# Optimization experiments

Measured on AMD Instinct MI355X. Metric: run time of the kernel, lower is better.

The kernel has to match this reference:

```python
import jax, jax.numpy as jnp
import numpy as np

DIM = 128
BASE = 10000.0
DIM_X = DIM // 2          # 64
DIM_Y = DIM - DIM_X       # 64
H = 512
W = 512


def setup_inputs() -> dict:
    key = jax.random.key(0)
    x = jax.random.normal(key, (1, H * W, DIM), dtype=jnp.float32)
    inv_freq_x = 1.0 / BASE ** (jnp.arange(0, DIM_X, 2, dtype=jnp.float32) / DIM_X)  # [DIM_X//2]
    inv_freq_y = 1.0 / BASE ** (jnp.arange(0, DIM_Y, 2, dtype=jnp.float32) / DIM_Y)  # [DIM_Y//2]
    return {"x": x, "inv_freq_x": inv_freq_x, "inv_freq_y": inv_freq_y,
            "height": H, "width": W}


def reference(x, inv_freq_x, inv_freq_y, height, width):
    dtype = x.dtype
    dim_x = 2 * inv_freq_x.shape[0]
    dim_y = 2 * inv_freq_y.shape[0]
    pos_x = jnp.arange(width, dtype=jnp.float32)   # [W]
    pos_y = jnp.arange(height, dtype=jnp.float32)  # [H]
    freqs_x = pos_x[:, None] * inv_freq_x[None, :]           # [W, dim_x//2]
    freqs_y = pos_y[:, None] * inv_freq_y[None, :]           # [H, dim_y//2]
    freqs_x = jnp.concatenate([freqs_x, freqs_x], axis=-1)   # [W, dim_x]
    freqs_y = jnp.concatenate([freqs_y, freqs_y], axis=-1)   # [H, dim_y]
    # first dim_x channels vary with w (broadcast over y); last dim_y vary with y
    cos_x = jnp.broadcast_to(jnp.cos(freqs_x).astype(dtype)[None, :, :], (height, width, dim_x))
    sin_x = jnp.broadcast_to(jnp.sin(freqs_x).astype(dtype)[None, :, :], (height, width, dim_x))
    cos_y = jnp.broadcast_to(jnp.cos(freqs_y).astype(dtype)[:, None, :], (height, width, dim_y))
    sin_y = jnp.broadcast_to(jnp.sin(freqs_y).astype(dtype)[:, None, :], (height, width, dim_y))
    cos_2d = jnp.concatenate([cos_x, cos_y], axis=-1).reshape(height * width, dim_x + dim_y)
    sin_2d = jnp.concatenate([sin_x, sin_y], axis=-1).reshape(height * width, dim_x + dim_y)
    return cos_2d, sin_2d
```

## Files before the change

kernel.cpp:

```cpp
#include <hip/hip_runtime.h>


typedef __attribute__((ext_vector_type(4))) float float4v;

__global__ __launch_bounds__(256) void rope2d_fast(
    const float* __restrict__ ifx,
    const float* __restrict__ ify,
    const int* __restrict__ wptr,
    float* __restrict__ out,
    int rows)
{
    const int idx = blockIdx.x * blockDim.x + threadIdx.x;
    const int total4 = rows << 6;
    if (idx >= total4) return;

    const int e = idx << 2;
    const int half = rows << 7;
    const bool is_sin = e >= half;
    const int e2 = is_sin ? e - half : e;

    const int p  = e2 >> 7;
    const int ch = e2 & 127;

    const int W = *wptr;
    int xw, yh;
    if ((W & (W - 1)) == 0) {
        const int s = __ffs(W) - 1;
        xw = p & (W - 1);
        yh = p >> s;
    } else {
        xw = p % W;
        yh = p / W;
    }

    const bool use_x = ch < 64;
    const float pos = use_x ? (float)xw : (float)yh;
    const float* tab = use_x ? ifx : ify;
    const float4v fr = *reinterpret_cast<const float4v*>(tab + (ch & 31));

    float4v v;
#pragma unroll
    for (int i = 0; i < 4; ++i) {
        const float f = pos * fr[i];
        v[i] = is_sin ? __sinf(f) : __cosf(f);
    }

    *reinterpret_cast<float4v*>(out + e) = v;
}

__global__ __launch_bounds__(256) void rope2d_generic(
    const float* __restrict__ ifx,
    const float* __restrict__ ify,
    const int* __restrict__ wptr,
    float* __restrict__ out,
    int rows, int dimx, int dimy)
{
    const int dim = dimx + dimy;
    const long long total = 2LL * rows * dim;
    const long long e = (long long)(blockIdx.x * blockDim.x + threadIdx.x);
    if (e >= total) return;

    const long long halfo = (long long)rows * dim;
    const bool is_sin = e >= halfo;
    const long long e2 = is_sin ? e - halfo : e;
    const int p  = (int)(e2 / dim);
    const int ch = (int)(e2 % dim);

    const int W = *wptr;
    const int xw = p % W, yh = p / W;

    float pos, f;
    if (ch < dimx) { pos = (float)xw; f = ifx[ch % (dimx >> 1)]; }
    else           { pos = (float)yh; f = ify[(ch - dimx) % (dimy >> 1)]; }
    const float ang = pos * f;
    out[e] = is_sin ? __sinf(ang) : __cosf(ang);
}

extern "C" void kernel_launch(void* const* d_in, const int* in_sizes, int n_in,
                              void* d_out, int out_size, void* d_ws, size_t ws_size,
                              hipStream_t stream) {
    const float* ifx = (const float*)d_in[1];
    const float* ify = (const float*)d_in[2];
    const int* wptr  = (const int*)d_in[4];
    float* out = (float*)d_out;

    const int dimx = 2 * in_sizes[1];
    const int dimy = 2 * in_sizes[2];
    const int dim  = dimx + dimy;
    const int rows = in_sizes[0] / dim;

    if (dimx == 64 && dimy == 64) {
        const int total4 = rows << 6;
        const int block = 256;
        const int grid = (total4 + block - 1) / block;
        rope2d_fast<<<grid, block, 0, stream>>>(ifx, ify, wptr, out, rows);
    } else {
        const long long total = 2LL * rows * dim;
        const int block = 256;
        const int grid = (int)((total + block - 1) / block);
        rope2d_generic<<<grid, block, 0, stream>>>(ifx, ify, wptr, out, rows, dimx, dimy);
    }
}
```

Baseline: 321.2 us.

## Precompute sin/cos tables in workspace and gather them in the fill kernel

New measurement: 320.3 us. About the same (-0.3%).

```diff
diff --git a/kernel.cpp b/kernel.cpp
--- a/kernel.cpp
+++ b/kernel.cpp
@@ -2,6 +2,81 @@
 
 
 typedef __attribute__((ext_vector_type(4))) float float4v;
+
+#define TABP  4096
+#define TABSZ (TABP * 32)
+
+__global__ __launch_bounds__(256) void rope2d_tables(
+    const float* __restrict__ ifx,
+    const float* __restrict__ ify,
+    float* __restrict__ ws)
+{
+    const int t = blockIdx.x * blockDim.x + threadIdx.x;
+    if (t >= TABSZ) return;
+    const float fp = (float)(t >> 5);
+    const int k = t & 31;
+    float sx, cx, sy, cy;
+    __sincosf(fp * ifx[k], &sx, &cx);
+    __sincosf(fp * ify[k], &sy, &cy);
+    ws[t]             = cx;
+    ws[TABSZ + t]     = sx;
+    ws[2 * TABSZ + t] = cy;
+    ws[3 * TABSZ + t] = sy;
+}
+
+__global__ __launch_bounds__(256) void rope2d_fill(
+    const float* __restrict__ ws,
+    const float* __restrict__ ifx,
+    const float* __restrict__ ify,
+    const int* __restrict__ wptr,
+    float* __restrict__ out,
+    int rows)
+{
+    const int idx = blockIdx.x * blockDim.x + threadIdx.x;
+    const int total4 = rows << 6;
+    if (idx >= total4) return;
+
+    const int e = idx << 2;
+    const int half = rows << 7;
+    const bool is_sin = e >= half;
+    const int e2 = is_sin ? e - half : e;
+
+    const int p  = e2 >> 7;
+    const int ch = e2 & 127;
+
+    const int W = *wptr;
+    int xw, yh;
+    if ((W & (W - 1)) == 0) {
+        const int s = __ffs(W) - 1;
+        xw = p & (W - 1);
+        yh = p >> s;
+    } else {
+        xw = p % W;
+        yh = p / W;
+    }
+
+    const bool use_x = ch < 64;
+    const int posi = use_x ? xw : yh;
+
+    float4v v;
+    if (posi < TABP) {
+        const int tsel = (is_sin ? 1 : 0) | (use_x ? 0 : 2);
+        const float* tab = ws + (size_t)tsel * TABSZ;
+        v = *reinterpret_cast<const float4v*>(tab + ((posi << 5) + (ch & 31)));
+    } else {
+        const float pos = (float)posi;
+        const float* ft = use_x ? ifx : ify;
+        const float4v fr = *reinterpret_cast<const float4v*>(ft + (ch & 31));
+#pragma unroll
+        for (int i = 0; i < 4; ++i) {
+            float s, c;
+            __sincosf(pos * fr[i], &s, &c);
+            v[i] = is_sin ? s : c;
+        }
+    }
+
+    *reinterpret_cast<float4v*>(out + e) = v;
+}
 
 __global__ __launch_bounds__(256) void rope2d_fast(
     const float* __restrict__ ifx,
@@ -89,11 +164,24 @@
     const int dim  = dimx + dimy;
     const int rows = in_sizes[0] / dim;
 
+    const size_t ws_needed = (size_t)4 * TABSZ * sizeof(float);
+
     if (dimx == 64 && dimy == 64) {
-        const int total4 = rows << 6;
-        const int block = 256;
-        const int grid = (total4 + block - 1) / block;
-        rope2d_fast<<<grid, block, 0, stream>>>(ifx, ify, wptr, out, rows);
+        if (d_ws != nullptr && ws_size >= ws_needed) {
+            float* ws = (float*)d_ws;
+            const int tb = 256;
+            const int tg = (TABSZ + tb - 1) / tb;
+            rope2d_tables<<<tg, tb, 0, stream>>>(ifx, ify, ws);
+            const int total4 = rows << 6;
+            const int block = 256;
+            const int grid = (total4 + block - 1) / block;
+            rope2d_fill<<<grid, block, 0, stream>>>(ws, ifx, ify, wptr, out, rows);
+        } else {
+            const int total4 = rows << 6;
+            const int block = 256;
+            const int grid = (total4 + block - 1) / block;
+            rope2d_fast<<<grid, block, 0, stream>>>(ifx, ify, wptr, out, rows);
+        }
     } else {
         const long long total = 2LL * rows * dim;
         const int block = 256;
```
